# Optimization experiments

Measured on AMD Instinct MI355X. Metric: run time of the kernel, lower is better.

Reference implementation:

```python
import jax, jax.numpy as jnp
import numpy as np

DIFF = 16  # static enlargement (max shake amplitude), offsets lie in [0, DIFF]


def setup_inputs() -> dict:
    key = jax.random.key(0)
    k1, k2, k3 = jax.random.split(key, 3)
    B, C, T, H, W = 8, 3, 32, 224, 224
    video = jax.random.uniform(k1, (B, C, T, H, W), dtype=jnp.float32)
    shake_h = jax.random.randint(k2, (T,), 0, DIFF + 1, dtype=jnp.int32)
    shake_w = jax.random.randint(k3, (T,), 0, DIFF + 1, dtype=jnp.int32)
    return {"video": video, "shake_h": shake_h, "shake_w": shake_w}


def reference(video, shake_h, shake_w):
    # Faithful jax version of Transform_Camera.forward_shake with the
    # randomly sampled shake curve provided as (already normalized)
    # per-frame integer offsets shake_h, shake_w in [0, DIFF].
    B, C, T, H, W = video.shape
    Hb, Wb = H + DIFF, W + DIFF
    # trilinear upsample over (T, H, W), half-pixel centers == torch align_corners=False
    enlarged = jax.image.resize(video, (B, C, T, Hb, Wb), method="trilinear")
    enlarged = jnp.clip(enlarged, 0.0, 1.0)

    def crop(frame, h, w):
        # frame: [B, C, Hb, Wb]; per-frame varying crop of size HxW
        return jax.lax.dynamic_slice(frame, (0, 0, h, w), (B, C, H, W))

    # vmap over the T axis replaces the python loop of crops + stack
    out = jax.vmap(crop, in_axes=(2, 0, 0), out_axes=2)(enlarged, shake_h, shake_w)
    return out  # [B, C, T, H, W]
```

## Files before the change

### kernel.cpp

```cpp
#include <hip/hip_runtime.h>

#define NB 8
#define NC 3
#define NT 32
#define NH 224
#define NW 224
#define DIFF 16
#define INV_SCALE (224.0f / 240.0f)

#define TILE_ROWS 16
#define TILES_PER_FRAME (NH / TILE_ROWS)
#define NFRAMES (NB * NC * NT)

__global__ __launch_bounds__(256) void shake_crop_global_kernel(
    const float* __restrict__ video,
    const int* __restrict__ shake_h,
    const int* __restrict__ shake_w,
    float* __restrict__ out)
{
    const int tid  = threadIdx.x;
    const int f    = blockIdx.x / TILES_PER_FRAME;
    const int tile = blockIdx.x - f * TILES_PER_FRAME;

    if (tid >= NW) return;

    const int t  = f % NT;
    const int sh = shake_h[t];
    const int sw = shake_w[t];
    const int ybase = tile * TILE_ROWS;

    const int x = tid;
    float ix = fminf(fmaxf((x + sw + 0.5f) * INV_SCALE - 0.5f, 0.0f), (float)(NW - 1));
    int   x0 = (int)ix;
    float fx = ix - (float)x0;
    int   x1 = min(x0 + 1, NW - 1);

    const float* frame = video + (size_t)f * (NH * NW);
    float* ocol = out + (size_t)f * (NH * NW) + (size_t)ybase * NW + x;
    const int ys = ybase + sh;

    #pragma unroll
    for (int ry = 0; ry < TILE_ROWS; ++ry) {
        float iy = fminf(fmaxf((ys + ry + 0.5f) * INV_SCALE - 0.5f, 0.0f), (float)(NH - 1));
        int   y0 = (int)iy;
        float fy = iy - (float)y0;
        int   y1 = min(y0 + 1, NH - 1);
        const float* r0p = frame + y0 * NW;
        const float* r1p = frame + y1 * NW;

        float v00 = r0p[x0];
        float v01 = r0p[x1];
        float v10 = r1p[x0];
        float v11 = r1p[x1];

        float top = v00 + fx * (v01 - v00);
        float bot = v10 + fx * (v11 - v10);
        float v   = top + fy * (bot - top);
        ocol[(size_t)ry * NW] = fminf(fmaxf(v, 0.0f), 1.0f);
    }
}

extern "C" void kernel_launch(void* const* d_in, const int* in_sizes, int n_in,
                              void* d_out, int out_size, void* d_ws, size_t ws_size,
                              hipStream_t stream) {
    const float* video   = (const float*)d_in[0];
    const int*   shake_h = (const int*)d_in[1];
    const int*   shake_w = (const int*)d_in[2];
    float*       out     = (float*)d_out;

    const int grid = NFRAMES * TILES_PER_FRAME;
    shake_crop_global_kernel<<<grid, 256, 0, stream>>>(video, shake_h, shake_w, out);
}
```

Before: 261.5 us.

## Vectorize crop kernel with float4 row loads, float2 stores and row reuse

Each thread now produces two adjacent output pixels. It loads one unaligned float4 per source row that covers both pixels' taps and keeps the previous bottom row in registers, so only one new row is loaded per output row. The block shrinks to 224 threads, split into two row groups of 8 rows each, with float2 stores. This cuts the number of load instructions and removes the 32 idle lanes per block, at the cost of select logic and unaligned vector loads.

```diff
diff --git a/kernel.cpp b/kernel.cpp
--- a/kernel.cpp
+++ b/kernel.cpp
@@ -11,8 +11,19 @@
 #define TILE_ROWS 16
 #define TILES_PER_FRAME (NH / TILE_ROWS)
 #define NFRAMES (NB * NC * NT)
+#define PAIRS (NW / 2)
+#define ROWG (TILE_ROWS / 2)
 
-__global__ __launch_bounds__(256) void shake_crop_global_kernel(
+typedef float float4a __attribute__((ext_vector_type(4), aligned(4)));
+
+__device__ __forceinline__ float pick4(float4a v, int r) {
+    float a = (r == 1) ? v.y : v.x;
+    a = (r == 2) ? v.z : a;
+    a = (r == 3) ? v.w : a;
+    return a;
+}
+
+__global__ __launch_bounds__(224) void shake_crop_vec_kernel(
     const float* __restrict__ video,
     const int* __restrict__ shake_h,
     const int* __restrict__ shake_w,
@@ -21,42 +32,69 @@
     const int tid  = threadIdx.x;
     const int f    = blockIdx.x / TILES_PER_FRAME;
     const int tile = blockIdx.x - f * TILES_PER_FRAME;
+    const int t    = f % NT;
+    const int sh   = shake_h[t];
+    const int sw   = shake_w[t];
+    const int ybase = tile * TILE_ROWS;
+    const int p = tid % PAIRS;
+    const int g = tid / PAIRS;
 
-    if (tid >= NW) return;
-
-    const int t  = f % NT;
-    const int sh = shake_h[t];
-    const int sw = shake_w[t];
-    const int ybase = tile * TILE_ROWS;
-
-    const int x = tid;
-    float ix = fminf(fmaxf((x + sw + 0.5f) * INV_SCALE - 0.5f, 0.0f), (float)(NW - 1));
-    int   x0 = (int)ix;
-    float fx = ix - (float)x0;
-    int   x1 = min(x0 + 1, NW - 1);
+    int x0j[2], x1j[2]; float fxj[2];
+    #pragma unroll
+    for (int j = 0; j < 2; ++j) {
+        int xo = p * 2 + j;
+        float ix = fminf(fmaxf((xo + sw + 0.5f) * INV_SCALE - 0.5f, 0.0f), (float)(NW - 1));
+        x0j[j] = (int)ix;
+        fxj[j] = ix - (float)x0j[j];
+        x1j[j] = min(x0j[j] + 1, NW - 1);
+    }
+    const int base = min(x0j[0], NW - 4);
+    const int r00 = x0j[0] - base, r01 = x1j[0] - base;
+    const int r10 = x0j[1] - base, r11 = x1j[1] - base;
 
     const float* frame = video + (size_t)f * (NH * NW);
-    float* ocol = out + (size_t)f * (NH * NW) + (size_t)ybase * NW + x;
-    const int ys = ybase + sh;
+    float2* orow = (float2*)(out + (size_t)f * (NH * NW)
+                                 + (size_t)(ybase + g * ROWG) * NW + p * 2);
+    const int ys = ybase + g * ROWG + sh;
+
+    float iyp = fminf(fmaxf((ys + 0.5f) * INV_SCALE - 0.5f, 0.0f), (float)(NH - 1));
+    const int pY0_init = (int)iyp;
+    float4a pr = *(const float4a*)(frame + pY0_init * NW + base);
+    float t00 = pick4(pr, r00), t01 = pick4(pr, r01);
+    float t10 = pick4(pr, r10), t11 = pick4(pr, r11);
+    float b00 = 0.f, b01 = 0.f, b10 = 0.f, b11 = 0.f;
+    int pY1 = -1;
 
     #pragma unroll
-    for (int ry = 0; ry < TILE_ROWS; ++ry) {
+    for (int ry = 0; ry < ROWG; ++ry) {
         float iy = fminf(fmaxf((ys + ry + 0.5f) * INV_SCALE - 0.5f, 0.0f), (float)(NH - 1));
         int   y0 = (int)iy;
         float fy = iy - (float)y0;
         int   y1 = min(y0 + 1, NH - 1);
-        const float* r0p = frame + y0 * NW;
-        const float* r1p = frame + y1 * NW;
 
-        float v00 = r0p[x0];
-        float v01 = r0p[x1];
-        float v10 = r1p[x0];
-        float v11 = r1p[x1];
+        const bool adv = (y0 == pY1);
+        float v00a = adv ? b00 : t00, v01a = adv ? b01 : t01;
+        float v10a = adv ? b10 : t10, v11a = adv ? b11 : t11;
 
-        float top = v00 + fx * (v01 - v00);
-        float bot = v10 + fx * (v11 - v10);
-        float v   = top + fy * (bot - top);
-        ocol[(size_t)ry * NW] = fminf(fmaxf(v, 0.0f), 1.0f);
+        float4a bot = *(const float4a*)(frame + y1 * NW + base);
+        float w00 = pick4(bot, r00), w01 = pick4(bot, r01);
+        float w10 = pick4(bot, r10), w11 = pick4(bot, r11);
+
+        float top0 = v00a + fxj[0] * (v01a - v00a);
+        float bot0 = w00  + fxj[0] * (w01  - w00);
+        float o0   = top0 + fy * (bot0 - top0);
+        float top1 = v10a + fxj[1] * (v11a - v10a);
+        float bot1 = w10  + fxj[1] * (w11  - w10);
+        float o1   = top1 + fy * (bot1 - top1);
+
+        float2 res;
+        res.x = fminf(fmaxf(o0, 0.0f), 1.0f);
+        res.y = fminf(fmaxf(o1, 0.0f), 1.0f);
+        orow[ry * (NW / 2)] = res;
+
+        t00 = v00a; t01 = v01a; t10 = v10a; t11 = v11a;
+        b00 = w00;  b01 = w01;  b10 = w10;  b11 = w11;
+        pY1 = y1;
     }
 }
 
@@ -69,5 +107,5 @@
     float*       out     = (float*)d_out;
 
     const int grid = NFRAMES * TILES_PER_FRAME;
-    shake_crop_global_kernel<<<grid, 256, 0, stream>>>(video, shake_h, shake_w, out);
+    shake_crop_vec_kernel<<<grid, 224, 0, stream>>>(video, shake_h, shake_w, out);
 }
```

Measured after the change: 266.1 us. About the same (+1.7%).
